# Performance work log

Hardware: AMD Instinct MI355X
Metric: run time of the kernel (lower is better)

The kernel has to match this reference:

```python
import jax, jax.numpy as jnp
import numpy as np

D_MODEL = 1024
D_STATE = 16
D_CONV = 4
EXPAND = 2
D_INNER = EXPAND * D_MODEL  # 2048
DT_RANK = 64  # ceil(d_model/16)
BATCH = 2
SEQLEN = 1024
DT_MIN, DT_MAX = 0.001, 0.1


def setup_inputs() -> dict:
    key = jax.random.key(0)
    ks = jax.random.split(key, 9)
    f = jnp.float32
    hidden_states = jax.random.normal(ks[0], (BATCH, SEQLEN, D_MODEL), f)
    in_proj_w = jax.random.normal(ks[1], (2 * D_INNER, D_MODEL), f) * 0.02
    conv_w = jax.random.normal(ks[2], (D_INNER, 1, D_CONV), f) * 0.1  # depthwise: (out, in/groups=1, kw)
    conv_b = jax.random.normal(ks[3], (D_INNER,), f) * 0.01
    x_proj_w = jax.random.normal(ks[4], (DT_RANK + 2 * D_STATE, D_INNER), f) * 0.02
    std = DT_RANK ** -0.5
    dt_proj_w = jax.random.uniform(ks[5], (D_INNER, DT_RANK), f, -std, std)
    dt = jnp.exp(jax.random.uniform(ks[6], (D_INNER,), f)
                 * (np.log(DT_MAX) - np.log(DT_MIN)) + np.log(DT_MIN))
    dt = jnp.clip(dt, 1e-4, None)
    dt_proj_b = dt + jnp.log(-jnp.expm1(-dt))  # inverse softplus, as in torch init
    A_log = jnp.log(jnp.tile(jnp.arange(1, D_STATE + 1, dtype=f), (D_INNER, 1)))  # [d_inner, d_state]
    D = jnp.ones((D_INNER,), f)
    out_proj_w = jax.random.normal(ks[7], (D_MODEL, D_INNER), f) * 0.02
    return dict(hidden_states=hidden_states, in_proj_w=in_proj_w, conv_w=conv_w,
                conv_b=conv_b, x_proj_w=x_proj_w, dt_proj_w=dt_proj_w,
                dt_proj_b=dt_proj_b, A_log=A_log, D=D, out_proj_w=out_proj_w)


def reference(hidden_states, in_proj_w, conv_w, conv_b, x_proj_w,
              dt_proj_w, dt_proj_b, A_log, D, out_proj_w):
    b = hidden_states.shape[0]
    # in_proj -> split into x and gate z
    xz = hidden_states @ in_proj_w.T                      # [b, l, 2*d_inner]
    x, z = jnp.split(xz, 2, axis=-1)                      # each [b, l, d_inner]
    # causal depthwise conv over time (torch pads both sides then drops the tail)
    xc = jnp.transpose(x, (0, 2, 1))                      # [b, d_inner, l]
    xp = jnp.pad(xc, ((0, 0), (0, 0), (D_CONV - 1, 0)))
    xc = jax.lax.conv_general_dilated(
        xp, conv_w, window_strides=(1,), padding='VALID',
        feature_group_count=D_INNER,
        dimension_numbers=('NCH', 'OIH', 'NCH')) + conv_b[None, :, None]
    u = jax.nn.silu(jnp.transpose(xc, (0, 2, 1)))         # [b, l, d_inner]
    # x_proj -> dt (low-rank), B, C
    x_dbl = u @ x_proj_w.T                                # [b, l, dt_rank + 2*d_state]
    dt_low, Bm, Cm = jnp.split(x_dbl, [DT_RANK, DT_RANK + D_STATE], axis=-1)
    delta = jax.nn.softplus(dt_low @ dt_proj_w.T + dt_proj_b)  # [b, l, d_inner]
    A = -jnp.exp(A_log)                                   # [d_inner, d_state]
    # discretize
    dA = jnp.exp(jnp.einsum('bld,dn->bldn', delta, A))    # [b, l, d_inner, d_state]
    dBu = (delta * u)[..., None] * Bm[:, :, None, :]      # [b, l, d_inner, d_state]
    # sequential selective scan over l
    xs = (jnp.moveaxis(dA, 1, 0), jnp.moveaxis(dBu, 1, 0), jnp.moveaxis(Cm, 1, 0))
    h0 = jnp.zeros((b, D_INNER, D_STATE), hidden_states.dtype)

    def step(h, inp):
        dA_t, dBu_t, C_t = inp
        h = dA_t * h + dBu_t                              # [b, d_inner, d_state]
        y_t = jnp.einsum('bdn,bn->bd', h, C_t)
        return h, y_t

    _, ys = jax.lax.scan(step, h0, xs)                    # ys: [l, b, d_inner]
    y = jnp.moveaxis(ys, 0, 1) + u * D                    # skip connection
    y = y * jax.nn.silu(z)                                # gate
    return y @ out_proj_w.T                               # [b, l, d_model]
```

## Files before the change

kernel.cpp:

```cpp
#include <hip/hip_runtime.h>
#include <hip/hip_bf16.h>
#include <math.h>

typedef __attribute__((ext_vector_type(8))) short short8;
typedef __attribute__((ext_vector_type(4))) float floatx4;
typedef unsigned short u16;
typedef unsigned int u32;

__device__ __forceinline__ float b2f(u16 v) {
    union { u32 i; float f; } x; x.i = ((u32)v) << 16; return x.f;
}
__device__ __forceinline__ u16 f2b(float f) {
    union { u32 i; float f; } x; x.f = f;
    u32 r = x.i + 0x7FFFu + ((x.i >> 16) & 1u);
    return (u16)(r >> 16);
}

__device__ __forceinline__ void gload_lds16(const u16* g, short* l) {
    __builtin_amdgcn_global_load_lds((const __attribute__((address_space(1))) void*)g,
                                     (__attribute__((address_space(3))) void*)l, 16, 0, 0);
}

#define BM 128
#define BN 128
#define BKg 64
#define NCHUNK 16
#define CT 64

__global__ void convert_all(const float* __restrict__ s0, u16* __restrict__ d0,
                            const float* __restrict__ s1, u16* __restrict__ d1,
                            const float* __restrict__ s2, u16* __restrict__ d2,
                            const float* __restrict__ s3, u16* __restrict__ d3,
                            const float* __restrict__ s4, u16* __restrict__ d4)
{
    int i = blockIdx.x * 256 + threadIdx.x;
    const float* src; u16* dst;
    if (i < 524288)            { src = s0; dst = d0; }
    else if (i < 1572864)      { src = s1; dst = d1; i -= 524288; }
    else if (i < 1622016)      { src = s2; dst = d2; i -= 1572864; }
    else if (i < 1654784)      { src = s3; dst = d3; i -= 1622016; }
    else if (i < 2179072)      { src = s4; dst = d4; i -= 1654784; }
    else return;
    float4 v = ((const float4*)src)[i];
    ushort4 o;
    o.x = f2b(v.x); o.y = f2b(v.y); o.z = f2b(v.z); o.w = f2b(v.w);
    ((ushort4*)dst)[i] = o;
}

template<int EPI, bool DMA>
__global__ __launch_bounds__(256, DMA ? 4 : 2)
void gemm_nt(const u16* __restrict__ A, const u16* __restrict__ B,
             void* __restrict__ Cout, const float* __restrict__ bias,
             int M, int N, int K_per_split, int lda, int ldb, int ldc)
{
    constexpr int LDW = BKg + (DMA ? 0 : 8);
    __shared__ __align__(16) short As[BM * LDW];
    __shared__ __align__(16) short Bs[BN * LDW];

    const int tid  = threadIdx.x;
    const int wave = tid >> 6;
    const int lane = tid & 63;
    const int m0 = blockIdx.x * BM;
    const int n0 = blockIdx.y * BN;
    const int k_begin = blockIdx.z * K_per_split;

    const int wm = (wave & 1) * 64;
    const int wn = (wave >> 1) * 64;

    floatx4 acc[4][4];
#pragma unroll
    for (int i = 0; i < 4; i++)
#pragma unroll
        for (int j = 0; j < 4; j++) acc[i][j] = (floatx4)(0.f);

    const int srow = wave * 32 + (lane >> 3);
    const int scol = (lane & 7) * 8;
    const int vrow = tid >> 1;
    const int vcol = (tid & 1) * 32;

    for (int k0 = 0; k0 < K_per_split; k0 += BKg) {
        const int kg = k_begin + k0;
        if constexpr (DMA) {
            __syncthreads();
#pragma unroll
            for (int j = 0; j < 4; j++) {
                const int r = srow + j * 8;
                gload_lds16(A + (size_t)(m0 + r) * lda + kg + scol, &As[r * LDW + scol]);
            }
#pragma unroll
            for (int j = 0; j < 4; j++) {
                const int r = srow + j * 8;
                if (n0 + r < N)
                    gload_lds16(B + (size_t)(n0 + r) * ldb + kg + scol, &Bs[r * LDW + scol]);
            }
            __syncthreads();
        } else {
            const u16* ag = A + (size_t)(m0 + vrow) * lda + kg + vcol;
            uint4 a0 = ((const uint4*)ag)[0];
            uint4 a1 = ((const uint4*)ag)[1];
            uint4 a2 = ((const uint4*)ag)[2];
            uint4 a3 = ((const uint4*)ag)[3];
            uint4 b0 = make_uint4(0,0,0,0), b1 = make_uint4(0,0,0,0);
            uint4 b2 = make_uint4(0,0,0,0), b3 = make_uint4(0,0,0,0);
            if (n0 + vrow < N) {
                const u16* bg = B + (size_t)(n0 + vrow) * ldb + kg + vcol;
                b0 = ((const uint4*)bg)[0];
                b1 = ((const uint4*)bg)[1];
                b2 = ((const uint4*)bg)[2];
                b3 = ((const uint4*)bg)[3];
            }
            __syncthreads();
            *(uint4*)&As[vrow * LDW + vcol]      = a0;
            *(uint4*)&As[vrow * LDW + vcol + 8]  = a1;
            *(uint4*)&As[vrow * LDW + vcol + 16] = a2;
            *(uint4*)&As[vrow * LDW + vcol + 24] = a3;
            *(uint4*)&Bs[vrow * LDW + vcol]      = b0;
            *(uint4*)&Bs[vrow * LDW + vcol + 8]  = b1;
            *(uint4*)&Bs[vrow * LDW + vcol + 16] = b2;
            *(uint4*)&Bs[vrow * LDW + vcol + 24] = b3;
            __syncthreads();
        }
#pragma unroll
        for (int kk = 0; kk < 2; kk++) {
            const int ko = kk * 32 + (lane >> 4) * 8;
            short8 af[4], bfr[4];
#pragma unroll
            for (int i = 0; i < 4; i++)
                af[i] = *(const short8*)&As[(wm + i * 16 + (lane & 15)) * LDW + ko];
#pragma unroll
            for (int j = 0; j < 4; j++)
                bfr[j] = *(const short8*)&Bs[(wn + j * 16 + (lane & 15)) * LDW + ko];
#pragma unroll
            for (int i = 0; i < 4; i++)
#pragma unroll
                for (int j = 0; j < 4; j++)
                    acc[i][j] = __builtin_amdgcn_mfma_f32_16x16x32_bf16(
                        af[i], bfr[j], acc[i][j], 0, 0, 0);
        }
    }

    const int cn0 = n0 + wn + (lane & 15);
    const int cm0 = m0 + wm + ((lane >> 4) << 2);
    const size_t zoff = (size_t)blockIdx.z * M * ldc;
#pragma unroll
    for (int i = 0; i < 4; i++) {
#pragma unroll
        for (int j = 0; j < 4; j++) {
            const int n = cn0 + j * 16;
            if (n < N) {
#pragma unroll
                for (int r = 0; r < 4; r++) {
                    const int m = cm0 + i * 16 + r;
                    float v = acc[i][j][r];
                    const size_t off = (size_t)m * ldc + n;
                    if constexpr (EPI == 1) {
                        ((u16*)Cout)[off] = f2b(v);
                    } else if constexpr (EPI == 6) {
                        v += bias[n];
                        float sp = (v > 15.f) ? v : log1pf(__expf(v));
                        ((u16*)Cout)[off] = f2b(sp);
                    } else {
                        ((float*)Cout)[zoff + off] = v;
                    }
                }
            }
        }
    }
}

__global__ void reduce_xdbl(const float* __restrict__ part, float* __restrict__ of,
                            u16* __restrict__ ob)
{
    const int i = blockIdx.x * 256 + threadIdx.x;
    if (i >= 49152) return;
    const size_t MN4 = 49152;
    float4 s = ((const float4*)part)[i];
#pragma unroll
    for (int z = 1; z < 16; z++) {
        const float4 p = ((const float4*)part)[z * MN4 + i];
        s.x += p.x; s.y += p.y; s.z += p.z; s.w += p.w;
    }
    ((float4*)of)[i] = s;
    ushort4 o;
    o.x = f2b(s.x); o.y = f2b(s.y); o.z = f2b(s.z); o.w = f2b(s.w);
    ((ushort4*)ob)[i] = o;
}

__global__ void reduce_out(const float* __restrict__ part, float* __restrict__ out)
{
    const int i = blockIdx.x * 256 + threadIdx.x;
    const size_t MN4 = 524288;
    float4 s = ((const float4*)part)[i];
#pragma unroll
    for (int z = 1; z < 4; z++) {
        const float4 p = ((const float4*)part)[z * MN4 + i];
        s.x += p.x; s.y += p.y; s.z += p.z; s.w += p.w;
    }
    ((float4*)out)[i] = s;
}

__global__ void conv_silu_kernel(const u16* __restrict__ xz, const float* __restrict__ cw,
                                 const float* __restrict__ cb, u16* __restrict__ u)
{
    const int idx = blockIdx.x * 256 + threadIdx.x;
    const int d = idx & 2047;
    const int row = idx >> 11;
    const int l = row & 1023;
    float acc = cb[d];
#pragma unroll
    for (int j = 0; j < 4; j++) {
        const int lj = l - 3 + j;
        if (lj >= 0)
            acc += cw[d * 4 + j] * b2f(xz[(size_t)(row - 3 + j) * 4096 + d]);
    }
    const float s = acc / (1.f + __expf(-acc));
    u[(size_t)row * 2048 + d] = f2b(s);
}

__global__ __launch_bounds__(256)
void scan_pass1(const u16* __restrict__ delta, const u16* __restrict__ u,
                const float* __restrict__ xdbl, const float* __restrict__ A_log,
                float* __restrict__ aP, float* __restrict__ hpart)
{
    __shared__ u16   dS[CT * 128];
    __shared__ u16   uS[CT * 128];
    __shared__ float BS[CT * 16];

    const int tid  = threadIdx.x;
    const int half = tid & 1;
    const int dloc = tid >> 1;
    const int d0 = blockIdx.x * 128;
    const int d = d0 + dloc;
    const int b = blockIdx.y >> 4;
    const int chunk = blockIdx.y & 15;
    const int bd = b * 2048 + d;
    const size_t row0 = (size_t)b * 1024 + chunk * CT;

    for (int i = tid; i < CT * 128 / 8; i += 256) {
        const int e = i * 8;
        const int t = e >> 7, c = e & 127;
        *(uint4*)&dS[e] = *(const uint4*)&delta[(row0 + t) * 2048 + d0 + c];
        *(uint4*)&uS[e] = *(const uint4*)&u[(row0 + t) * 2048 + d0 + c];
    }
    for (int i = tid; i < CT * 16; i += 256) {
        const int t = i >> 4, n = i & 15;
        BS[i] = xdbl[(row0 + t) * 96 + 64 + n];
    }

    float A_dn[8], h[8], ap[8];
#pragma unroll
    for (int j = 0; j < 8; j++) {
        A_dn[j] = -__expf(A_log[d * 16 + half * 8 + j]);
        h[j] = 0.f; ap[j] = 1.f;
    }
    __syncthreads();

#pragma unroll 4
    for (int t = 0; t < CT; t++) {
        const float dl = b2f(dS[t * 128 + dloc]);
        const float uu = b2f(uS[t * 128 + dloc]);
        const float dlu = dl * uu;
        const float4 B0 = *(const float4*)&BS[t * 16 + half * 8];
        const float4 B1 = *(const float4*)&BS[t * 16 + half * 8 + 4];
        const float Bv[8] = {B0.x, B0.y, B0.z, B0.w, B1.x, B1.y, B1.z, B1.w};
#pragma unroll
        for (int j = 0; j < 8; j++) {
            const float dA = __expf(dl * A_dn[j]);
            h[j] = dA * h[j] + dlu * Bv[j];
            ap[j] *= dA;
        }
    }

    const size_t o = ((size_t)(bd * 16 + chunk) * 16) + half * 8;
    *(float4*)&aP[o]     = make_float4(ap[0], ap[1], ap[2], ap[3]);
    *(float4*)&aP[o + 4] = make_float4(ap[4], ap[5], ap[6], ap[7]);
    *(float4*)&hpart[o]     = make_float4(h[0], h[1], h[2], h[3]);
    *(float4*)&hpart[o + 4] = make_float4(h[4], h[5], h[6], h[7]);
}

__global__ void scan_combine(const float* __restrict__ aP, float* __restrict__ hp)
{
    const int idx = blockIdx.x * 256 + threadIdx.x;
    const int n = idx & 15;
    const int bd = idx >> 4;
    float h = 0.f;
    for (int c = 0; c < NCHUNK; c++) {
        const size_t o = ((size_t)(bd * 16 + c) * 16) + n;
        const float a = aP[o];
        const float p = hp[o];
        hp[o] = h;
        h = a * h + p;
    }
}

__global__ __launch_bounds__(256)
void scan_pass2(const u16* __restrict__ delta, const u16* __restrict__ u,
                const float* __restrict__ xdbl, const u16* __restrict__ xz,
                const float* __restrict__ A_log, const float* __restrict__ Dv,
                const float* __restrict__ hinit, u16* __restrict__ ybuf)
{
    __shared__ u16   dS[CT * 128];
    __shared__ u16   uS[CT * 128];
    __shared__ u16   zS[CT * 128];
    __shared__ float BS[CT * 16];
    __shared__ float CS[CT * 16];

    const int tid  = threadIdx.x;
    const int half = tid & 1;
    const int dloc = tid >> 1;
    const int d0 = blockIdx.x * 128;
    const int d = d0 + dloc;
    const int b = blockIdx.y >> 4;
    const int chunk = blockIdx.y & 15;
    const int bd = b * 2048 + d;
    const size_t row0 = (size_t)b * 1024 + chunk * CT;

    for (int i = tid; i < CT * 128 / 8; i += 256) {
        const int e = i * 8;
        const int t = e >> 7, c = e & 127;
        *(uint4*)&dS[e] = *(const uint4*)&delta[(row0 + t) * 2048 + d0 + c];
        *(uint4*)&uS[e] = *(const uint4*)&u[(row0 + t) * 2048 + d0 + c];
        *(uint4*)&zS[e] = *(const uint4*)&xz[(row0 + t) * 4096 + 2048 + d0 + c];
    }
    for (int i = tid; i < CT * 16; i += 256) {
        const int t = i >> 4, n = i & 15;
        BS[i] = xdbl[(row0 + t) * 96 + 64 + n];
        CS[i] = xdbl[(row0 + t) * 96 + 80 + n];
    }

    const size_t o = ((size_t)(bd * 16 + chunk) * 16) + half * 8;
    const float4 h0 = *(const float4*)&hinit[o];
    const float4 h1 = *(const float4*)&hinit[o + 4];
    float h[8] = {h0.x, h0.y, h0.z, h0.w, h1.x, h1.y, h1.z, h1.w};
    float A_dn[8];
#pragma unroll
    for (int j = 0; j < 8; j++)
        A_dn[j] = -__expf(A_log[d * 16 + half * 8 + j]);
    const float Dd = Dv[d];
    __syncthreads();

#pragma unroll 4
    for (int t = 0; t < CT; t++) {
        const float dl = b2f(dS[t * 128 + dloc]);
        const float uu = b2f(uS[t * 128 + dloc]);
        const float dlu = dl * uu;
        const float4 B0 = *(const float4*)&BS[t * 16 + half * 8];
        const float4 B1 = *(const float4*)&BS[t * 16 + half * 8 + 4];
        const float4 C0 = *(const float4*)&CS[t * 16 + half * 8];
        const float4 C1 = *(const float4*)&CS[t * 16 + half * 8 + 4];
        const float Bv[8] = {B0.x, B0.y, B0.z, B0.w, B1.x, B1.y, B1.z, B1.w};
        const float Cv[8] = {C0.x, C0.y, C0.z, C0.w, C1.x, C1.y, C1.z, C1.w};
        float p = 0.f;
#pragma unroll
        for (int j = 0; j < 8; j++) {
            const float dA = __expf(dl * A_dn[j]);
            h[j] = dA * h[j] + dlu * Bv[j];
            p += h[j] * Cv[j];
        }
        p += __shfl_xor(p, 1);
        if (half == 0) {
            const float z = b2f(zS[t * 128 + dloc]);
            const float gt = z / (1.f + __expf(-z));
            ybuf[(row0 + t) * 2048 + d] = f2b((p + uu * Dd) * gt);
        }
    }
}

extern "C" void kernel_launch(void* const* d_in, const int* in_sizes, int n_in,
                              void* d_out, int out_size, void* d_ws, size_t ws_size,
                              hipStream_t stream)
{
    const float* hid    = (const float*)d_in[0];
    const float* w_in   = (const float*)d_in[1];
    const float* conv_w = (const float*)d_in[2];
    const float* conv_b = (const float*)d_in[3];
    const float* w_x    = (const float*)d_in[4];
    const float* w_dt   = (const float*)d_in[5];
    const float* b_dt   = (const float*)d_in[6];
    const float* A_log  = (const float*)d_in[7];
    const float* Dvec   = (const float*)d_in[8];
    const float* w_out  = (const float*)d_in[9];
    float* out = (float*)d_out;

    const size_t MB = 1048576;
    char* ws = (char*)d_ws;
    u16*   xz     = (u16*)(ws + 0);
    u16*   ubuf   = (u16*)(ws + 16 * MB);
    float* part3  = (float*)(ws + 24 * MB);
    u16*   delta  = (u16*)(ws + 24 * MB);
    float* part6  = (float*)(ws + 0);
    float* xdblf  = (float*)(ws + 40 * MB);
    u16*   xdblb  = (u16*)(ws + 40 * MB + 786432);
    u16*   w_x_b  = (u16*)(ws + 41 * MB + 131072);
    u16*   w_dt_b = (u16*)(ws + 41 * MB + 524288);
    u16*   hid_b  = (u16*)(ws + 42 * MB);
    float* hpart  = (float*)(ws + 42 * MB);
    u16*   w_in_b = (u16*)(ws + 46 * MB);
    float* aP     = (float*)(ws + 50 * MB);
    u16*   ybuf   = (u16*)(ws + 46 * MB);
    u16*   w_out_b= (u16*)(ws + 54 * MB);

    convert_all<<<8512, 256, 0, stream>>>(hid, hid_b, w_in, w_in_b, w_x, w_x_b,
                                          w_dt, w_dt_b, w_out, w_out_b);

    gemm_nt<1, true><<<dim3(16, 32, 1), 256, 0, stream>>>(hid_b, w_in_b, xz, nullptr,
                                                          2048, 4096, 1024, 1024, 1024, 4096);
    conv_silu_kernel<<<16384, 256, 0, stream>>>(xz, conv_w, conv_b, ubuf);
    gemm_nt<5, false><<<dim3(16, 1, 16), 256, 0, stream>>>(ubuf, w_x_b, part3, nullptr,
                                                           2048, 96, 128, 2048, 2048, 96);
    reduce_xdbl<<<192, 256, 0, stream>>>(part3, xdblf, xdblb);
    gemm_nt<6, false><<<dim3(16, 16, 1), 256, 0, stream>>>(xdblb, w_dt_b, delta, b_dt,
                                                           2048, 2048, 64, 96, 64, 2048);
    scan_pass1<<<dim3(16, 32), 256, 0, stream>>>(delta, ubuf, xdblf, A_log, aP, hpart);
    scan_combine<<<256, 256, 0, stream>>>(aP, hpart);
    scan_pass2<<<dim3(16, 32), 256, 0, stream>>>(delta, ubuf, xdblf, xz, A_log, Dvec,
                                                 hpart, ybuf);
    gemm_nt<5, true><<<dim3(16, 8, 4), 256, 0, stream>>>(ybuf, w_out_b, part6, nullptr,
                                                         2048, 1024, 512, 2048, 2048, 1024);
    reduce_out<<<2048, 256, 0, stream>>>(part6, out);
}
```

Measured before the change: 260.5 us.

## Fuse dt projection GEMM into scan passes and fold chunk combine into pass2

Removes the standalone dt_proj GEMM and computes delta per chunk inside both scan passes using MFMA on LDS tiles of xdbl and the dt weights, with softplus applied in place. The scan_combine kernel is dropped: pass2 serially folds earlier chunk prefixes from aP/hpart itself. B/C now come from the bf16 xdbl instead of an fp32 copy, and the conv kernel is vectorised to four channels per thread. This saves launches and the delta round-trip through global memory, at the cost of computing the dt GEMM twice and doing redundant per-chunk prefix work in pass2.

```diff
diff --git a/kernel.cpp b/kernel.cpp
--- a/kernel.cpp
+++ b/kernel.cpp
@@ -50,8 +50,8 @@
 template<int EPI, bool DMA>
 __global__ __launch_bounds__(256, DMA ? 4 : 2)
 void gemm_nt(const u16* __restrict__ A, const u16* __restrict__ B,
-             void* __restrict__ Cout, const float* __restrict__ bias,
-             int M, int N, int K_per_split, int lda, int ldb, int ldc)
+             void* __restrict__ Cout, int M, int N, int K_per_split,
+             int lda, int ldb, int ldc)
 {
     constexpr int LDW = BKg + (DMA ? 0 : 8);
     __shared__ __align__(16) short As[BM * LDW];
@@ -155,10 +155,6 @@
                     const size_t off = (size_t)m * ldc + n;
                     if constexpr (EPI == 1) {
                         ((u16*)Cout)[off] = f2b(v);
-                    } else if constexpr (EPI == 6) {
-                        v += bias[n];
-                        float sp = (v > 15.f) ? v : log1pf(__expf(v));
-                        ((u16*)Cout)[off] = f2b(sp);
                     } else {
                         ((float*)Cout)[zoff + off] = v;
                     }
@@ -168,8 +164,7 @@
     }
 }
 
-__global__ void reduce_xdbl(const float* __restrict__ part, float* __restrict__ of,
-                            u16* __restrict__ ob)
+__global__ void reduce_xdbl(const float* __restrict__ part, u16* __restrict__ ob)
 {
     const int i = blockIdx.x * 256 + threadIdx.x;
     if (i >= 49152) return;
@@ -180,7 +175,6 @@
         const float4 p = ((const float4*)part)[z * MN4 + i];
         s.x += p.x; s.y += p.y; s.z += p.z; s.w += p.w;
     }
-    ((float4*)of)[i] = s;
     ushort4 o;
     o.x = f2b(s.x); o.y = f2b(s.y); o.z = f2b(s.z); o.w = f2b(s.w);
     ((ushort4*)ob)[i] = o;
@@ -203,28 +197,70 @@
                                  const float* __restrict__ cb, u16* __restrict__ u)
 {
     const int idx = blockIdx.x * 256 + threadIdx.x;
-    const int d = idx & 2047;
-    const int row = idx >> 11;
+    const int d = (idx & 511) * 4;
+    const int row = idx >> 9;
     const int l = row & 1023;
-    float acc = cb[d];
+    const float4 cbv = *(const float4*)&cb[d];
+    float acc[4] = {cbv.x, cbv.y, cbv.z, cbv.w};
 #pragma unroll
     for (int j = 0; j < 4; j++) {
         const int lj = l - 3 + j;
-        if (lj >= 0)
-            acc += cw[d * 4 + j] * b2f(xz[(size_t)(row - 3 + j) * 4096 + d]);
-    }
-    const float s = acc / (1.f + __expf(-acc));
-    u[(size_t)row * 2048 + d] = f2b(s);
+        if (lj >= 0) {
+            const ushort4 xv = *(const ushort4*)&xz[(size_t)(row - 3 + j) * 4096 + d];
+            acc[0] += cw[(d + 0) * 4 + j] * b2f(xv.x);
+            acc[1] += cw[(d + 1) * 4 + j] * b2f(xv.y);
+            acc[2] += cw[(d + 2) * 4 + j] * b2f(xv.z);
+            acc[3] += cw[(d + 3) * 4 + j] * b2f(xv.w);
+        }
+    }
+    ushort4 o;
+    o.x = f2b(acc[0] / (1.f + __expf(-acc[0])));
+    o.y = f2b(acc[1] / (1.f + __expf(-acc[1])));
+    o.z = f2b(acc[2] / (1.f + __expf(-acc[2])));
+    o.w = f2b(acc[3] / (1.f + __expf(-acc[3])));
+    *(ushort4*)&u[(size_t)row * 2048 + d] = o;
+}
+
+
+#define DLD 132
+
+__device__ __forceinline__ void dt_gemm(const u16* xdtS, const u16* wdtS, u16* dS,
+                                        const float* bias, int d0, int tid)
+{
+    const int wave = tid >> 6, lane = tid & 63;
+    const int tw = wave * 16;
+    const short8 af0 = *(const short8*)&xdtS[(tw + (lane & 15)) * 72 + (lane >> 4) * 8];
+    const short8 af1 = *(const short8*)&xdtS[(tw + (lane & 15)) * 72 + 32 + (lane >> 4) * 8];
+#pragma unroll
+    for (int dt = 0; dt < 8; dt++) {
+        const short8 b0 = *(const short8*)&wdtS[(dt * 16 + (lane & 15)) * 72 + (lane >> 4) * 8];
+        const short8 b1 = *(const short8*)&wdtS[(dt * 16 + (lane & 15)) * 72 + 32 + (lane >> 4) * 8];
+        floatx4 a = (floatx4)(0.f);
+        a = __builtin_amdgcn_mfma_f32_16x16x32_bf16(af0, b0, a, 0, 0, 0);
+        a = __builtin_amdgcn_mfma_f32_16x16x32_bf16(af1, b1, a, 0, 0, 0);
+        const int dd = dt * 16 + (lane & 15);
+        const float bs = bias[d0 + dd];
+#pragma unroll
+        for (int r = 0; r < 4; r++) {
+            const int tt = tw + ((lane >> 4) << 2) + r;
+            const float v = a[r] + bs;
+            const float sp = (v > 15.f) ? v : log1pf(__expf(v));
+            dS[tt * DLD + dd] = f2b(sp);
+        }
+    }
 }
 
 __global__ __launch_bounds__(256)
-void scan_pass1(const u16* __restrict__ delta, const u16* __restrict__ u,
-                const float* __restrict__ xdbl, const float* __restrict__ A_log,
+void scan_pass1(const u16* __restrict__ xdblb, const u16* __restrict__ wdt,
+                const float* __restrict__ bias, const u16* __restrict__ u,
+                const float* __restrict__ A_log,
                 float* __restrict__ aP, float* __restrict__ hpart)
 {
-    __shared__ u16   dS[CT * 128];
-    __shared__ u16   uS[CT * 128];
-    __shared__ float BS[CT * 16];
+    __shared__ __align__(16) u16 xdtS[64 * 72];
+    __shared__ __align__(16) u16 wdtS[128 * 72];
+    __shared__ __align__(16) u16 dS[CT * DLD];
+    __shared__ __align__(16) u16 uS[CT * 128];
+    __shared__ __align__(16) float BSf[CT * 16];
 
     const int tid  = threadIdx.x;
     const int half = tid & 1;
@@ -236,15 +272,27 @@
     const int bd = b * 2048 + d;
     const size_t row0 = (size_t)b * 1024 + chunk * CT;
 
-    for (int i = tid; i < CT * 128 / 8; i += 256) {
+    for (int i = tid; i < 512; i += 256) {
+        const int t = i >> 3, c = (i & 7) * 8;
+        *(uint4*)&xdtS[t * 72 + c] = *(const uint4*)&xdblb[(row0 + t) * 96 + c];
+    }
+    for (int i = tid; i < 1024; i += 256) {
+        const int r = i >> 3, c = (i & 7) * 8;
+        *(uint4*)&wdtS[r * 72 + c] = *(const uint4*)&wdt[(size_t)(d0 + r) * 64 + c];
+    }
+    for (int i = tid; i < 1024; i += 256) {
         const int e = i * 8;
         const int t = e >> 7, c = e & 127;
-        *(uint4*)&dS[e] = *(const uint4*)&delta[(row0 + t) * 2048 + d0 + c];
         *(uint4*)&uS[e] = *(const uint4*)&u[(row0 + t) * 2048 + d0 + c];
     }
-    for (int i = tid; i < CT * 16; i += 256) {
-        const int t = i >> 4, n = i & 15;
-        BS[i] = xdbl[(row0 + t) * 96 + 64 + n];
+    if (tid < 128) {
+        const int t = tid >> 1, c = (tid & 1) * 8;
+        const ushort4 lo = *(const ushort4*)&xdblb[(row0 + t) * 96 + 64 + c];
+        const ushort4 hi = *(const ushort4*)&xdblb[(row0 + t) * 96 + 64 + c + 4];
+        BSf[t * 16 + c + 0] = b2f(lo.x); BSf[t * 16 + c + 1] = b2f(lo.y);
+        BSf[t * 16 + c + 2] = b2f(lo.z); BSf[t * 16 + c + 3] = b2f(lo.w);
+        BSf[t * 16 + c + 4] = b2f(hi.x); BSf[t * 16 + c + 5] = b2f(hi.y);
+        BSf[t * 16 + c + 6] = b2f(hi.z); BSf[t * 16 + c + 7] = b2f(hi.w);
     }
 
     float A_dn[8], h[8], ap[8];
@@ -254,14 +302,16 @@
         h[j] = 0.f; ap[j] = 1.f;
     }
     __syncthreads();
+    dt_gemm(xdtS, wdtS, dS, bias, d0, tid);
+    __syncthreads();
 
 #pragma unroll 4
     for (int t = 0; t < CT; t++) {
-        const float dl = b2f(dS[t * 128 + dloc]);
+        const float dl = b2f(dS[t * DLD + dloc]);
         const float uu = b2f(uS[t * 128 + dloc]);
         const float dlu = dl * uu;
-        const float4 B0 = *(const float4*)&BS[t * 16 + half * 8];
-        const float4 B1 = *(const float4*)&BS[t * 16 + half * 8 + 4];
+        const float4 B0 = *(const float4*)&BSf[t * 16 + half * 8];
+        const float4 B1 = *(const float4*)&BSf[t * 16 + half * 8 + 4];
         const float Bv[8] = {B0.x, B0.y, B0.z, B0.w, B1.x, B1.y, B1.z, B1.w};
 #pragma unroll
         for (int j = 0; j < 8; j++) {
@@ -278,32 +328,21 @@
     *(float4*)&hpart[o + 4] = make_float4(h[4], h[5], h[6], h[7]);
 }
 
-__global__ void scan_combine(const float* __restrict__ aP, float* __restrict__ hp)
-{
-    const int idx = blockIdx.x * 256 + threadIdx.x;
-    const int n = idx & 15;
-    const int bd = idx >> 4;
-    float h = 0.f;
-    for (int c = 0; c < NCHUNK; c++) {
-        const size_t o = ((size_t)(bd * 16 + c) * 16) + n;
-        const float a = aP[o];
-        const float p = hp[o];
-        hp[o] = h;
-        h = a * h + p;
-    }
-}
-
 __global__ __launch_bounds__(256)
-void scan_pass2(const u16* __restrict__ delta, const u16* __restrict__ u,
-                const float* __restrict__ xdbl, const u16* __restrict__ xz,
-                const float* __restrict__ A_log, const float* __restrict__ Dv,
-                const float* __restrict__ hinit, u16* __restrict__ ybuf)
-{
-    __shared__ u16   dS[CT * 128];
-    __shared__ u16   uS[CT * 128];
-    __shared__ u16   zS[CT * 128];
-    __shared__ float BS[CT * 16];
-    __shared__ float CS[CT * 16];
+void scan_pass2(const u16* __restrict__ xdblb, const u16* __restrict__ wdt,
+                const float* __restrict__ bias, const u16* __restrict__ u,
+                const u16* __restrict__ xz, const float* __restrict__ A_log,
+                const float* __restrict__ Dv, const float* __restrict__ aP,
+                const float* __restrict__ hpart, u16* __restrict__ ybuf)
+{
+    __shared__ __align__(16) u16 unionS[64 * 72 + 128 * 72];
+    __shared__ __align__(16) u16 dS[CT * DLD];
+    __shared__ __align__(16) u16 uS[CT * 128];
+    __shared__ __align__(16) float BSf[CT * 16];
+    __shared__ __align__(16) float CSf[CT * 16];
+    u16* xdtS = unionS;
+    u16* wdtS = unionS + 64 * 72;
+    u16* zS   = unionS;
 
     const int tid  = threadIdx.x;
     const int half = tid & 1;
@@ -315,39 +354,76 @@
     const int bd = b * 2048 + d;
     const size_t row0 = (size_t)b * 1024 + chunk * CT;
 
-    for (int i = tid; i < CT * 128 / 8; i += 256) {
+    uint4 zreg[4];
+#pragma unroll
+    for (int k = 0; k < 4; k++) {
+        const int e = (tid + k * 256) * 8;
+        const int t = e >> 7, c = e & 127;
+        zreg[k] = *(const uint4*)&xz[(row0 + t) * 4096 + 2048 + d0 + c];
+    }
+
+    for (int i = tid; i < 512; i += 256) {
+        const int t = i >> 3, c = (i & 7) * 8;
+        *(uint4*)&xdtS[t * 72 + c] = *(const uint4*)&xdblb[(row0 + t) * 96 + c];
+    }
+    for (int i = tid; i < 1024; i += 256) {
+        const int r = i >> 3, c = (i & 7) * 8;
+        *(uint4*)&wdtS[r * 72 + c] = *(const uint4*)&wdt[(size_t)(d0 + r) * 64 + c];
+    }
+    for (int i = tid; i < 1024; i += 256) {
         const int e = i * 8;
         const int t = e >> 7, c = e & 127;
-        *(uint4*)&dS[e] = *(const uint4*)&delta[(row0 + t) * 2048 + d0 + c];
         *(uint4*)&uS[e] = *(const uint4*)&u[(row0 + t) * 2048 + d0 + c];
-        *(uint4*)&zS[e] = *(const uint4*)&xz[(row0 + t) * 4096 + 2048 + d0 + c];
-    }
-    for (int i = tid; i < CT * 16; i += 256) {
-        const int t = i >> 4, n = i & 15;
-        BS[i] = xdbl[(row0 + t) * 96 + 64 + n];
-        CS[i] = xdbl[(row0 + t) * 96 + 80 + n];
-    }
-
-    const size_t o = ((size_t)(bd * 16 + chunk) * 16) + half * 8;
-    const float4 h0 = *(const float4*)&hinit[o];
-    const float4 h1 = *(const float4*)&hinit[o + 4];
-    float h[8] = {h0.x, h0.y, h0.z, h0.w, h1.x, h1.y, h1.z, h1.w};
+    }
+    if (tid < 128) {
+        const int t = tid >> 1, c = (tid & 1) * 8;
+#pragma unroll
+        for (int q = 0; q < 8; q++) {
+            BSf[t * 16 + c + q] = b2f(xdblb[(row0 + t) * 96 + 64 + c + q]);
+            CSf[t * 16 + c + q] = b2f(xdblb[(row0 + t) * 96 + 80 + c + q]);
+        }
+    }
+
+    float h[8];
+#pragma unroll
+    for (int j = 0; j < 8; j++) h[j] = 0.f;
+    for (int c = 0; c < chunk; c++) {
+        const size_t o = ((size_t)(bd * 16 + c) * 16) + half * 8;
+        const float4 a0 = *(const float4*)&aP[o];
+        const float4 a1 = *(const float4*)&aP[o + 4];
+        const float4 p0 = *(const float4*)&hpart[o];
+        const float4 p1 = *(const float4*)&hpart[o + 4];
+        h[0] = a0.x * h[0] + p0.x; h[1] = a0.y * h[1] + p0.y;
+        h[2] = a0.z * h[2] + p0.z; h[3] = a0.w * h[3] + p0.w;
+        h[4] = a1.x * h[4] + p1.x; h[5] = a1.y * h[5] + p1.y;
+        h[6] = a1.z * h[6] + p1.z; h[7] = a1.w * h[7] + p1.w;
+    }
+
     float A_dn[8];
 #pragma unroll
     for (int j = 0; j < 8; j++)
         A_dn[j] = -__expf(A_log[d * 16 + half * 8 + j]);
     const float Dd = Dv[d];
+
+    __syncthreads();
+    dt_gemm(xdtS, wdtS, dS, bias, d0, tid);
+    __syncthreads();
+#pragma unroll
+    for (int k = 0; k < 4; k++) {
+        const int e = (tid + k * 256) * 8;
+        *(uint4*)&zS[e] = zreg[k];
+    }
     __syncthreads();
 
 #pragma unroll 4
     for (int t = 0; t < CT; t++) {
-        const float dl = b2f(dS[t * 128 + dloc]);
+        const float dl = b2f(dS[t * DLD + dloc]);
         const float uu = b2f(uS[t * 128 + dloc]);
         const float dlu = dl * uu;
-        const float4 B0 = *(const float4*)&BS[t * 16 + half * 8];
-        const float4 B1 = *(const float4*)&BS[t * 16 + half * 8 + 4];
-        const float4 C0 = *(const float4*)&CS[t * 16 + half * 8];
-        const float4 C1 = *(const float4*)&CS[t * 16 + half * 8 + 4];
+        const float4 B0 = *(const float4*)&BSf[t * 16 + half * 8];
+        const float4 B1 = *(const float4*)&BSf[t * 16 + half * 8 + 4];
+        const float4 C0 = *(const float4*)&CSf[t * 16 + half * 8];
+        const float4 C1 = *(const float4*)&CSf[t * 16 + half * 8 + 4];
         const float Bv[8] = {B0.x, B0.y, B0.z, B0.w, B1.x, B1.y, B1.z, B1.w};
         const float Cv[8] = {C0.x, C0.y, C0.z, C0.w, C1.x, C1.y, C1.z, C1.w};
         float p = 0.f;
@@ -387,35 +463,30 @@
     u16*   xz     = (u16*)(ws + 0);
     u16*   ubuf   = (u16*)(ws + 16 * MB);
     float* part3  = (float*)(ws + 24 * MB);
-    u16*   delta  = (u16*)(ws + 24 * MB);
+    float* aP     = (float*)(ws + 32 * MB);
+    float* hpart  = (float*)(ws + 36 * MB);
     float* part6  = (float*)(ws + 0);
-    float* xdblf  = (float*)(ws + 40 * MB);
-    u16*   xdblb  = (u16*)(ws + 40 * MB + 786432);
-    u16*   w_x_b  = (u16*)(ws + 41 * MB + 131072);
-    u16*   w_dt_b = (u16*)(ws + 41 * MB + 524288);
+    u16*   xdblb  = (u16*)(ws + 40 * MB);
+    u16*   w_x_b  = (u16*)(ws + 40 * MB + 524288);
+    u16*   w_dt_b = (u16*)(ws + 41 * MB);
     u16*   hid_b  = (u16*)(ws + 42 * MB);
-    float* hpart  = (float*)(ws + 42 * MB);
     u16*   w_in_b = (u16*)(ws + 46 * MB);
-    float* aP     = (float*)(ws + 50 * MB);
     u16*   ybuf   = (u16*)(ws + 46 * MB);
     u16*   w_out_b= (u16*)(ws + 54 * MB);
 
     convert_all<<<8512, 256, 0, stream>>>(hid, hid_b, w_in, w_in_b, w_x, w_x_b,
                                           w_dt, w_dt_b, w_out, w_out_b);
-
-    gemm_nt<1, true><<<dim3(16, 32, 1), 256, 0, stream>>>(hid_b, w_in_b, xz, nullptr,
+    gemm_nt<1, true><<<dim3(16, 32, 1), 256, 0, stream>>>(hid_b, w_in_b, xz,
                                                           2048, 4096, 1024, 1024, 1024, 4096);
-    conv_silu_kernel<<<16384, 256, 0, stream>>>(xz, conv_w, conv_b, ubuf);
-    gemm_nt<5, false><<<dim3(16, 1, 16), 256, 0, stream>>>(ubuf, w_x_b, part3, nullptr,
+    conv_silu_kernel<<<4096, 256, 0, stream>>>(xz, conv_w, conv_b, ubuf);
+    gemm_nt<5, false><<<dim3(16, 1, 16), 256, 0, stream>>>(ubuf, w_x_b, part3,
                                                            2048, 96, 128, 2048, 2048, 96);
-    reduce_xdbl<<<192, 256, 0, stream>>>(part3, xdblf, xdblb);
-    gemm_nt<6, false><<<dim3(16, 16, 1), 256, 0, stream>>>(xdblb, w_dt_b, delta, b_dt,
-                                                           2048, 2048, 64, 96, 64, 2048);
-    scan_pass1<<<dim3(16, 32), 256, 0, stream>>>(delta, ubuf, xdblf, A_log, aP, hpart);
-    scan_combine<<<256, 256, 0, stream>>>(aP, hpart);
-    scan_pass2<<<dim3(16, 32), 256, 0, stream>>>(delta, ubuf, xdblf, xz, A_log, Dvec,
-                                                 hpart, ybuf);
-    gemm_nt<5, true><<<dim3(16, 8, 4), 256, 0, stream>>>(ybuf, w_out_b, part6, nullptr,
+    reduce_xdbl<<<192, 256, 0, stream>>>(part3, xdblb);
+    scan_pass1<<<dim3(16, 32), 256, 0, stream>>>(xdblb, w_dt_b, b_dt, ubuf, A_log,
+                                                 aP, hpart);
+    scan_pass2<<<dim3(16, 32), 256, 0, stream>>>(xdblb, w_dt_b, b_dt, ubuf, xz, A_log,
+                                                 Dvec, aP, hpart, ybuf);
+    gemm_nt<5, true><<<dim3(16, 8, 4), 256, 0, stream>>>(ybuf, w_out_b, part6,
                                                          2048, 1024, 512, 2048, 2048, 1024);
     reduce_out<<<2048, 256, 0, stream>>>(part6, out);
 }
```

Result: slower. 274.8 us (+5.5%).
